# Optimization experiments

Hardware: AMD Instinct MI355X
Metric: run time of the kernel (lower is better)

The kernel has to match this reference:

```python
import jax, jax.numpy as jnp
import numpy as np

EPS = 1e-6

def setup_inputs() -> dict:
    key = jax.random.key(0)
    kX, ky, kl, kg, ks, kp = jax.random.split(key, 6)
    B, T, N = 65536, 512, 5000
    X = jax.random.randint(kX, (B, 4), 0, N, dtype=jnp.int32)
    y = jax.random.randint(ky, (B, T), 0, 2, dtype=jnp.int32)
    learn_w = jax.random.normal(kl, (N, 1), dtype=jnp.float32)
    guess_w = jax.random.normal(kg, (N, 1), dtype=jnp.float32)
    slip_w = jax.random.normal(ks, (N, 1), dtype=jnp.float32)
    prior_w = jax.random.normal(kp, (N, 1), dtype=jnp.float32)
    return {"X": X, "y": y, "learn_w": learn_w, "guess_w": guess_w,
            "slip_w": slip_w, "prior_w": prior_w}

def _bkt_forward(X, y, learn_w, guess_w, slip_w, prior_w):
    # per-student BKT parameters, each (B,)
    l = jax.nn.sigmoid(learn_w[X[:, 0], 0])
    g = jax.nn.sigmoid(guess_w[X[:, 1], 0])
    s = jax.nn.sigmoid(slip_w[X[:, 2], 0])
    p = jax.nn.sigmoid(prior_w[X[:, 3], 0])
    y_obs = jnp.where(y == -1, 0, y).astype(l.dtype)  # (B, T), -1 padding -> 0

    def step(latent, y_t):
        # latent: (B,) mastery prob at time t (recorded BEFORE update)
        correct = latent * (1 - s) + (1 - latent) * g
        k_t1 = latent * (1 - s) / correct
        k_t0 = latent * s / (latent * s + (1 - latent) * (1 - g))
        k_t = jnp.where(y_t > 0.5, k_t1, k_t0)
        next_latent = jnp.clip(k_t + (1 - k_t) * l, EPS, 1 - EPS)
        return next_latent, (correct, latent)

    _, (corrects, latents) = jax.lax.scan(step, p, y_obs.T)  # scan over T
    return corrects.T, latents.T  # (B, T) each

def reference(X, y, learn_w, guess_w, slip_w, prior_w):
    return _bkt_forward(X, y, learn_w, guess_w, slip_w, prior_w)
```

## Files before the change

kernel.cpp:

```cpp
#include <hip/hip_runtime.h>
#include <cmath>


#define LSTR 36

__device__ __forceinline__ int comp4(const int4& v, int c) {
    return c == 0 ? v.x : c == 1 ? v.y : c == 2 ? v.z : v.w;
}

__global__ __launch_bounds__(256, 1) void bkt_fwd(
    const int* __restrict__ X,
    const int* __restrict__ Y,
    const float* __restrict__ learn_w,
    const float* __restrict__ guess_w,
    const float* __restrict__ slip_w,
    const float* __restrict__ prior_w,
    float* __restrict__ out,
    int B, int T)
{
#pragma clang fp contract(off)
    const int tid = threadIdx.x;
    const int b = blockIdx.x * 256 + tid;

    __shared__ float xp[256 * LSTR];

    const int4 xi = *reinterpret_cast<const int4*>(X + (size_t)b * 4);
    const float l = (float)(1.0 / (1.0 + exp(-(double)learn_w[xi.x])));
    const float g = (float)(1.0 / (1.0 + exp(-(double)guess_w[xi.y])));
    const float s = (float)(1.0 / (1.0 + exp(-(double)slip_w[xi.z])));
    const float p = (float)(1.0 / (1.0 + exp(-(double)prior_w[xi.w])));

    const float oms = 1.0f - s;
    const float omg = 1.0f - g;
    const float lo  = 1e-6f;
    const float hi  = (float)(1.0 - 1e-6);
    float latent = p;

    const int4* __restrict__ yv = reinterpret_cast<const int4*>(Y + (size_t)b * T);

    const int wv = tid >> 6, ln = tid & 63;
    const int r8 = ln >> 3, c8 = ln & 7;
    float* __restrict__ lrow = xp + tid * LSTR;
    const float* __restrict__ lrd = xp + (wv * 64 + r8) * LSTR + c8 * 4;
    float* __restrict__ gco = out + (size_t)(blockIdx.x * 256 + wv * 64 + r8) * T + c8 * 4;
    float* __restrict__ gla = gco + (size_t)B * T;

    constexpr int STEPS = 32, NQ = 8;
    const int nOuter = T / STEPS;

    int4 yq[NQ], yqn[NQ];
    #pragma unroll
    for (int q = 0; q < NQ; ++q) yq[q] = yv[q];

    for (int o = 0; o < nOuter; ++o) {
        if (o + 1 < nOuter) {
            #pragma unroll
            for (int q = 0; q < NQ; ++q) yqn[q] = yv[(o + 1) * NQ + q];
        }

        float cr[STEPS], lt[STEPS];
        #pragma unroll
        for (int j = 0; j < STEPS; ++j) {
            const float a       = latent * oms;
            const float omlat   = 1.0f - latent;
            const float t1      = omlat * g;
            const float correct = a + t1;
            const float n0      = latent * s;
            const float t2      = omlat * omg;
            const float d0      = n0 + t2;
            const bool hit = comp4(yq[j >> 2], j & 3) > 0;
            const float num = hit ? a : n0;
            const float den = hit ? correct : d0;
            const float k   = num / den;
            cr[j] = correct;
            lt[j] = latent;
            const float omk = 1.0f - k;
            const float t3  = omk * l;
            const float nxt = k + t3;
            latent = fminf(fmaxf(nxt, lo), hi);
        }

        const int colo = o * STEPS;

        #pragma unroll
        for (int q = 0; q < NQ; ++q)
            *reinterpret_cast<float4*>(lrow + q * 4) =
                make_float4(cr[4*q], cr[4*q+1], cr[4*q+2], cr[4*q+3]);
        __builtin_amdgcn_wave_barrier();
        #pragma unroll
        for (int q = 0; q < NQ; ++q) {
            const float4 v = *reinterpret_cast<const float4*>(lrd + (q * 8) * LSTR);
            *reinterpret_cast<float4*>(gco + (size_t)(q * 8) * T + colo) = v;
        }
        __builtin_amdgcn_wave_barrier();

        #pragma unroll
        for (int q = 0; q < NQ; ++q)
            *reinterpret_cast<float4*>(lrow + q * 4) =
                make_float4(lt[4*q], lt[4*q+1], lt[4*q+2], lt[4*q+3]);
        __builtin_amdgcn_wave_barrier();
        #pragma unroll
        for (int q = 0; q < NQ; ++q) {
            const float4 v = *reinterpret_cast<const float4*>(lrd + (q * 8) * LSTR);
            *reinterpret_cast<float4*>(gla + (size_t)(q * 8) * T + colo) = v;
        }
        __builtin_amdgcn_wave_barrier();

        #pragma unroll
        for (int q = 0; q < NQ; ++q) yq[q] = yqn[q];
    }
}

extern "C" void kernel_launch(void* const* d_in, const int* in_sizes, int n_in,
                              void* d_out, int out_size, void* d_ws, size_t ws_size,
                              hipStream_t stream)
{
    const int*   X  = (const int*)d_in[0];
    const int*   Y  = (const int*)d_in[1];
    const float* lw = (const float*)d_in[2];
    const float* gw = (const float*)d_in[3];
    const float* sw = (const float*)d_in[4];
    const float* pw = (const float*)d_in[5];
    float* out = (float*)d_out;

    const int B = in_sizes[0] / 4;
    const int T = in_sizes[1] / B;

    const int threads = 256;
    const int blocks = B / threads;
    bkt_fwd<<<blocks, threads, 0, stream>>>(X, Y, lw, gw, sw, pw, out, B, T);
}
```

Measured before the change: 89.98 us.

## Overlap previous chunk's output stores with current recurrence steps via swizzled LDS

Instead of computing a 32-step chunk and then doing a serialized LDS transpose plus global store for corrects and latents, the kernel writes both arrays to a 64-float-per-row XOR-swizzled LDS buffer. It then drains the previous chunk's global stores interleaved inside the next chunk's recurrence loop. The next y loads are also spread across the steps. This aims to hide store and LDS latency behind the dependent-division recurrence and to cut barrier and bank-conflict overhead. The cost is a larger LDS footprint (64KB per block) and more register and instruction pressure inside the hot loop.

```diff
diff --git a/kernel.cpp b/kernel.cpp
--- a/kernel.cpp
+++ b/kernel.cpp
@@ -1,8 +1,6 @@
 #include <hip/hip_runtime.h>
 #include <cmath>
 
-
-#define LSTR 36
 
 __device__ __forceinline__ int comp4(const int4& v, int c) {
     return c == 0 ? v.x : c == 1 ? v.y : c == 2 ? v.z : v.w;
@@ -22,7 +20,7 @@
     const int tid = threadIdx.x;
     const int b = blockIdx.x * 256 + tid;
 
-    __shared__ float xp[256 * LSTR];
+    __shared__ float xp[256 * 64];
 
     const int4 xi = *reinterpret_cast<const int4*>(X + (size_t)b * 4);
     const float l = (float)(1.0 / (1.0 + exp(-(double)learn_w[xi.x])));
@@ -39,11 +37,10 @@
     const int4* __restrict__ yv = reinterpret_cast<const int4*>(Y + (size_t)b * T);
 
     const int wv = tid >> 6, ln = tid & 63;
-    const int r8 = ln >> 3, c8 = ln & 7;
-    float* __restrict__ lrow = xp + tid * LSTR;
-    const float* __restrict__ lrd = xp + (wv * 64 + r8) * LSTR + c8 * 4;
-    float* __restrict__ gco = out + (size_t)(blockIdx.x * 256 + wv * 64 + r8) * T + c8 * 4;
-    float* __restrict__ gla = gco + (size_t)B * T;
+    const int r8 = ln >> 3;
+    const int s8 = ln & 7;
+    float* __restrict__ gcoB = out + (size_t)(blockIdx.x * 256 + wv * 64 + r8) * T + s8 * 4;
+    float* __restrict__ glaB = gcoB + (size_t)B * T;
 
     constexpr int STEPS = 32, NQ = 8;
     const int nOuter = T / STEPS;
@@ -53,14 +50,16 @@
     for (int q = 0; q < NQ; ++q) yq[q] = yv[q];
 
     for (int o = 0; o < nOuter; ++o) {
-        if (o + 1 < nOuter) {
-            #pragma unroll
-            for (int q = 0; q < NQ; ++q) yqn[q] = yv[(o + 1) * NQ + q];
-        }
+        const bool hasPrev = (o > 0);
+        const bool hasNext = (o + 1 < nOuter);
+        const int colPrev = (o - 1) * STEPS;
 
         float cr[STEPS], lt[STEPS];
         #pragma unroll
         for (int j = 0; j < STEPS; ++j) {
+            if ((j & 3) == 0 && hasNext)
+                yqn[j >> 2] = yv[(o + 1) * NQ + (j >> 2)];
+
             const float a       = latent * oms;
             const float omlat   = 1.0f - latent;
             const float t1      = omlat * g;
@@ -78,36 +77,56 @@
             const float t3  = omk * l;
             const float nxt = k + t3;
             latent = fminf(fmaxf(nxt, lo), hi);
+
+            if ((j & 1) == 1 && hasPrev) {
+                const int idx = j >> 1;
+                if (idx < NQ) {
+                    const int q  = idx;
+                    const int rl = wv * 64 + q * 8 + r8;
+                    const float4 v = *reinterpret_cast<const float4*>(
+                        xp + rl * 64 + ((s8 ^ (rl & 7)) << 2));
+                    *reinterpret_cast<float4*>(gcoB + (size_t)(q * 8) * T + colPrev) = v;
+                } else {
+                    const int q  = idx - NQ;
+                    const int rl = wv * 64 + q * 8 + r8;
+                    const float4 v = *reinterpret_cast<const float4*>(
+                        xp + rl * 64 + ((8 + (s8 ^ (rl & 7))) << 2));
+                    *reinterpret_cast<float4*>(glaB + (size_t)(q * 8) * T + colPrev) = v;
+                }
+            }
         }
 
-        const int colo = o * STEPS;
-
+        __builtin_amdgcn_wave_barrier();
         #pragma unroll
         for (int q = 0; q < NQ; ++q)
-            *reinterpret_cast<float4*>(lrow + q * 4) =
+            *reinterpret_cast<float4*>(xp + tid * 64 + ((q ^ (tid & 7)) << 2)) =
                 make_float4(cr[4*q], cr[4*q+1], cr[4*q+2], cr[4*q+3]);
-        __builtin_amdgcn_wave_barrier();
         #pragma unroll
-        for (int q = 0; q < NQ; ++q) {
-            const float4 v = *reinterpret_cast<const float4*>(lrd + (q * 8) * LSTR);
-            *reinterpret_cast<float4*>(gco + (size_t)(q * 8) * T + colo) = v;
-        }
+        for (int q = 0; q < NQ; ++q)
+            *reinterpret_cast<float4*>(xp + tid * 64 + ((8 + (q ^ (tid & 7))) << 2)) =
+                make_float4(lt[4*q], lt[4*q+1], lt[4*q+2], lt[4*q+3]);
         __builtin_amdgcn_wave_barrier();
 
-        #pragma unroll
-        for (int q = 0; q < NQ; ++q)
-            *reinterpret_cast<float4*>(lrow + q * 4) =
-                make_float4(lt[4*q], lt[4*q+1], lt[4*q+2], lt[4*q+3]);
-        __builtin_amdgcn_wave_barrier();
-        #pragma unroll
-        for (int q = 0; q < NQ; ++q) {
-            const float4 v = *reinterpret_cast<const float4*>(lrd + (q * 8) * LSTR);
-            *reinterpret_cast<float4*>(gla + (size_t)(q * 8) * T + colo) = v;
+        if (hasNext) {
+            #pragma unroll
+            for (int q = 0; q < NQ; ++q) yq[q] = yqn[q];
         }
-        __builtin_amdgcn_wave_barrier();
+    }
 
-        #pragma unroll
-        for (int q = 0; q < NQ; ++q) yq[q] = yqn[q];
+    const int colLast = (nOuter - 1) * STEPS;
+    #pragma unroll
+    for (int q = 0; q < NQ; ++q) {
+        const int rl = wv * 64 + q * 8 + r8;
+        const float4 v = *reinterpret_cast<const float4*>(
+            xp + rl * 64 + ((s8 ^ (rl & 7)) << 2));
+        *reinterpret_cast<float4*>(gcoB + (size_t)(q * 8) * T + colLast) = v;
+    }
+    #pragma unroll
+    for (int q = 0; q < NQ; ++q) {
+        const int rl = wv * 64 + q * 8 + r8;
+        const float4 v = *reinterpret_cast<const float4*>(
+            xp + rl * 64 + ((8 + (s8 ^ (rl & 7))) << 2));
+        *reinterpret_cast<float4*>(glaB + (size_t)(q * 8) * T + colLast) = v;
     }
 }
 
```

Measured after the change: 96.21 us. +6.9%, slower.
